# Kernel optimization log

Hardware: AMD Instinct MI355X
Metric: run time of the kernel (lower is better)

Reference implementation:

```python
import jax, jax.numpy as jnp
import numpy as np

B = 4
S = 2_000_000
NPIX = 196608  # 12 * 128**2 (HEALPix nside=128)


def setup_inputs() -> dict:
    key = jax.random.key(0)
    k1, k2, k3, k4 = jax.random.split(key, 4)
    tod = jax.random.normal(k1, (B, S), dtype=jnp.float32)
    # per-sample Stokes weights (I, Q, U) of the pointing matrix rows
    weights = jax.random.normal(k2, (S, 3), dtype=jnp.float32)
    projection_cov = jax.random.uniform(k3, (NPIX,), dtype=jnp.float32)
    pix_idx = jax.random.randint(k4, (S,), 0, NPIX, dtype=jnp.int32)
    return {"tod": tod, "weights": weights, "projection_cov": projection_cov,
            "pix_idx": pix_idx}


def reference(tod, weights, projection_cov, pix_idx):
    npix = projection_cov.shape[0]
    # P^T: scatter-add each TOD sample's Stokes contribution into its pixel.
    # contrib: [B, S, 3]
    contrib = tod[:, :, None] * weights[None, :, :]
    sky = jax.vmap(
        lambda c: jax.ops.segment_sum(c, pix_idx, num_segments=npix)
    )(contrib)  # [B, npix, 3]
    # coverage normalization of I, Q, U
    sky = sky / projection_cov[None, :, None]
    return sky
```

## Files before the change

### kernel.cpp

```cpp
#include <hip/hip_runtime.h>


constexpr int NB   = 768;
constexpr int BW   = 256;
constexpr int NBLK = 512;
constexpr int TILE = 2048;


__device__ __forceinline__ unsigned f2bf(float f) {
    unsigned u = __float_as_uint(f);
    unsigned r = ((u >> 16) & 1u) + 0x7fffu;
    return (u + r) >> 16;
}
__device__ __forceinline__ float bf_lo(unsigned u) {
    return __uint_as_float(u << 16);
}
__device__ __forceinline__ float bf_hi(unsigned u) {
    return __uint_as_float(u & 0xffff0000u);
}


__global__ __launch_bounds__(512)
void hist_kernel(const int* __restrict__ pix, int S, int chunk,
                 int* __restrict__ hist2d) {
    __shared__ int lh[NB];
    for (int t = threadIdx.x; t < NB; t += blockDim.x) lh[t] = 0;
    __syncthreads();
    const int beg = blockIdx.x * chunk;
    const int end = min(S, beg + chunk);
    for (int j = beg + threadIdx.x; j < end; j += blockDim.x)
        atomicAdd(&lh[pix[j] >> 8], 1);
    __syncthreads();
    for (int t = threadIdx.x; t < NB; t += blockDim.x)
        hist2d[(size_t)blockIdx.x * NB + t] = lh[t];
}

__global__ __launch_bounds__(NBLK)
void scan_blocks_kernel(int* __restrict__ hist2d,
                        int* __restrict__ btotal) {
    __shared__ int sc[NBLK];
    const int bkt = blockIdx.x, tid = threadIdx.x;
    const int v = hist2d[(size_t)tid * NB + bkt];
    sc[tid] = v;
    __syncthreads();
    for (int off = 1; off < NBLK; off <<= 1) {
        int x = (tid >= off) ? sc[tid - off] : 0;
        __syncthreads();
        sc[tid] += x;
        __syncthreads();
    }
    hist2d[(size_t)tid * NB + bkt] = sc[tid] - v;
    if (tid == NBLK - 1) btotal[bkt] = sc[tid];
}

__global__ void scan_buckets_kernel(const int* __restrict__ btotal,
                                    int* __restrict__ bbase, int S) {
    __shared__ int sc[NB];
    const int tid = threadIdx.x;
    const int v = btotal[tid];
    sc[tid] = v;
    __syncthreads();
    for (int off = 1; off < NB; off <<= 1) {
        int x = (tid >= off) ? sc[tid - off] : 0;
        __syncthreads();
        sc[tid] += x;
        __syncthreads();
    }
    bbase[tid] = sc[tid] - v;
    if (tid == NB - 1) bbase[NB] = sc[tid];
}

__global__ __launch_bounds__(1024)
void reorder_payload_kernel(const float* __restrict__ tod,
                            const float* __restrict__ weights,
                            const int* __restrict__ pix,
                            int S, int chunk,
                            const int* __restrict__ hist2d,
                            const int* __restrict__ bbase,
                            uint4* __restrict__ rec) {
    __shared__ int lbase[NB];
    __shared__ int lcur[NB];
    const int blk = blockIdx.x;
    for (int t = threadIdx.x; t < NB; t += blockDim.x) {
        lbase[t] = bbase[t] + hist2d[(size_t)blk * NB + t];
        lcur[t] = 0;
    }
    __syncthreads();
    const int beg = blk * chunk;
    const int end = min(S, beg + chunk);
    const int bs  = blockDim.x;

    int j = beg + (int)threadIdx.x;
    int p = 0;
    float w0 = 0, w1 = 0, w2 = 0, t0 = 0, t1 = 0, t2 = 0, t3 = 0;
    if (j < end) {
        p  = pix[j];
        w0 = weights[3 * j + 0]; w1 = weights[3 * j + 1]; w2 = weights[3 * j + 2];
        t0 = tod[(size_t)0 * S + j]; t1 = tod[(size_t)1 * S + j];
        t2 = tod[(size_t)2 * S + j]; t3 = tod[(size_t)3 * S + j];
    }
    while (j < end) {
        const int jn = j + bs;
        int pn = 0;
        float wn0 = 0, wn1 = 0, wn2 = 0, tn0 = 0, tn1 = 0, tn2 = 0, tn3 = 0;
        if (jn < end) {
            pn  = pix[jn];
            wn0 = weights[3 * jn + 0]; wn1 = weights[3 * jn + 1]; wn2 = weights[3 * jn + 2];
            tn0 = tod[(size_t)0 * S + jn]; tn1 = tod[(size_t)1 * S + jn];
            tn2 = tod[(size_t)2 * S + jn]; tn3 = tod[(size_t)3 * S + jn];
        }
        const int bkt = p >> 8;
        const int r   = atomicAdd(&lcur[bkt], 1);
        const int dst = lbase[bkt] + r;
        uint4 v;
        v.x = f2bf(w0) | (f2bf(w1) << 16);
        v.y = f2bf(w2) | ((unsigned)(p & (BW - 1)) << 16);
        v.z = f2bf(t0) | (f2bf(t1) << 16);
        v.w = f2bf(t2) | (f2bf(t3) << 16);
        rec[dst] = v;
        j = jn; p = pn;
        w0 = wn0; w1 = wn1; w2 = wn2;
        t0 = tn0; t1 = tn1; t2 = tn2; t3 = tn3;
    }
}

__global__ __launch_bounds__(1024)
void accum_sort_kernel(const uint4* __restrict__ rec,
                       const float* __restrict__ cov,
                       const int* __restrict__ bbase,
                       float* __restrict__ out,
                       int npix) {
    __shared__ uint4          lrec[TILE];
    __shared__ int            lp[TILE];
    __shared__ unsigned short lidx[TILE];
    __shared__ int            start[BW + 1];
    __shared__ int            cur[BW];

    const int bkt = blockIdx.x;
    const int beg = bbase[bkt], end = bbase[bkt + 1];
    const int l = threadIdx.x & (BW - 1);
    const int q = threadIdx.x >> 8;
    float s0 = 0.f, s1 = 0.f, s2 = 0.f;

    for (int tbeg = beg; tbeg < end; tbeg += TILE) {
        const int n = min(TILE, end - tbeg);

        if (threadIdx.x < BW) cur[threadIdx.x] = 0;
        for (int j = threadIdx.x; j < n; j += blockDim.x) {
            const uint4 r = rec[(size_t)(tbeg + j)];
            lrec[j] = r;
            lp[j]   = (int)(r.y >> 16);
        }
        __syncthreads();

        for (int j = threadIdx.x; j < n; j += blockDim.x)
            atomicAdd(&cur[lp[j]], 1);
        __syncthreads();

        if (threadIdx.x < 64) {
            const int i0 = threadIdx.x * 4;
            const int a0 = cur[i0], a1 = cur[i0 + 1];
            const int a2 = cur[i0 + 2], a3 = cur[i0 + 3];
            const int t1 = a0 + a1, t2 = t1 + a2, t3 = t2 + a3;
            int x = t3;
            #pragma unroll
            for (int off = 1; off < 64; off <<= 1) {
                const int y = __shfl_up(x, off, 64);
                if ((int)threadIdx.x >= off) x += y;
            }
            const int base = x - t3;
            start[i0]     = base;
            start[i0 + 1] = base + a0;
            start[i0 + 2] = base + t1;
            start[i0 + 3] = base + t2;
            if (threadIdx.x == 63) start[BW] = base + t3;
            cur[i0]     = base;
            cur[i0 + 1] = base + a0;
            cur[i0 + 2] = base + t1;
            cur[i0 + 3] = base + t2;
        }
        __syncthreads();

        for (int j = threadIdx.x; j < n; j += blockDim.x) {
            const int r = atomicAdd(&cur[lp[j]], 1);
            lidx[r] = (unsigned short)j;
        }
        __syncthreads();

        const int rb = start[l], re = start[l + 1];
        for (int j = rb; j < re; ++j) {
            const int i = lidx[j];
            const uint4 r = lrec[i];
            float tq;
            if      (q == 0) tq = bf_lo(r.z);
            else if (q == 1) tq = bf_hi(r.z);
            else if (q == 2) tq = bf_lo(r.w);
            else             tq = bf_hi(r.w);
            s0 += tq * bf_lo(r.x);
            s1 += tq * bf_hi(r.x);
            s2 += tq * bf_lo(r.y);
        }
        __syncthreads();
    }

    const int p = bkt * BW + l;
    const float rc = 1.0f / cov[p];
    const size_t o = ((size_t)q * npix + p) * 3;
    out[o + 0] = s0 * rc;
    out[o + 1] = s1 * rc;
    out[o + 2] = s2 * rc;
}


__global__ void zero_out_kernel(float4* __restrict__ out, int n4) {
    int i = blockIdx.x * blockDim.x + threadIdx.x;
    int stride = gridDim.x * blockDim.x;
    for (; i < n4; i += stride) out[i] = make_float4(0.f, 0.f, 0.f, 0.f);
}

__global__ void scatter_kernel(const float* __restrict__ tod,
                               const float* __restrict__ weights,
                               const int*   __restrict__ pix,
                               float* __restrict__ out,
                               int S, int npix, int B) {
    int i = blockIdx.x * blockDim.x + threadIdx.x;
    int stride = gridDim.x * blockDim.x;
    const size_t bstride = (size_t)npix * 3;
    for (int s = i; s < S; s += stride) {
        const int p = pix[s];
        const float w0 = weights[3 * s + 0];
        const float w1 = weights[3 * s + 1];
        const float w2 = weights[3 * s + 2];
        float* o = out + (size_t)p * 3;
        for (int b = 0; b < B; ++b) {
            const float t = tod[(size_t)b * S + s];
            float* ob = o + (size_t)b * bstride;
            atomicAdd(ob + 0, t * w0);
            atomicAdd(ob + 1, t * w1);
            atomicAdd(ob + 2, t * w2);
        }
    }
}

__global__ void normalize_kernel(float* __restrict__ out,
                                 const float* __restrict__ cov,
                                 int npix, int B) {
    int i = blockIdx.x * blockDim.x + threadIdx.x;
    int stride = gridDim.x * blockDim.x;
    const int total = B * npix;
    for (; i < total; i += stride) {
        const int p = i % npix;
        const float c = cov[p];
        float* o = out + (size_t)i * 3;
        o[0] /= c; o[1] /= c; o[2] /= c;
    }
}


extern "C" void kernel_launch(void* const* d_in, const int* in_sizes, int n_in,
                              void* d_out, int out_size, void* d_ws, size_t ws_size,
                              hipStream_t stream) {
    const float* tod     = (const float*)d_in[0];
    const float* weights = (const float*)d_in[1];
    const float* cov     = (const float*)d_in[2];
    const int*   pix     = (const int*)d_in[3];
    float* out = (float*)d_out;

    const int S    = in_sizes[3];
    const int npix = in_sizes[2];
    const int B    = in_sizes[0] / S;

    const size_t meta_ints  = (size_t)NB * NBLK + NB + (NB + 1);
    const size_t meta_bytes = ((meta_ints * sizeof(int)) + 63) & ~(size_t)63;
    const size_t need_rec   = meta_bytes + (size_t)S * 16;

    const int chunk = (S + NBLK - 1) / NBLK;

    if (B == 4 && npix == NB * BW && ws_size >= need_rec) {
        int* hist2d = (int*)d_ws;
        int* btotal = hist2d + (size_t)NB * NBLK;
        int* bbase  = btotal + NB;
        uint4* rec  = (uint4*)((char*)d_ws + meta_bytes);

        hist_kernel<<<NBLK, 512, 0, stream>>>(pix, S, chunk, hist2d);
        scan_blocks_kernel<<<NB, NBLK, 0, stream>>>(hist2d, btotal);
        scan_buckets_kernel<<<1, NB, 0, stream>>>(btotal, bbase, S);
        reorder_payload_kernel<<<NBLK, 1024, 0, stream>>>(tod, weights, pix, S,
                                                          chunk, hist2d, bbase, rec);
        accum_sort_kernel<<<NB, 1024, 0, stream>>>(rec, cov, bbase, out, npix);
        return;
    }

    const int block = 256;
    {
        const int n4 = out_size / 4;
        int grid = min((n4 + block - 1) / block, 2048);
        zero_out_kernel<<<grid, block, 0, stream>>>((float4*)out, n4);
    }
    {
        int grid = min((S + block - 1) / block, 4096);
        scatter_kernel<<<grid, block, 0, stream>>>(tod, weights, pix, out, S, npix, B);
    }
    {
        const int total = B * npix;
        int grid = min((total + block - 1) / block, 2048);
        normalize_kernel<<<grid, block, 0, stream>>>(out, cov, npix, B);
    }
}
```

Baseline: 72.99 us.

## Use wider pixel buckets and locally sort records before global scatter

Buckets change from 768×256 pixels to 256×768 pixels, and the number of reorder chunks doubles to 1024, each at most one TILE. The reorder kernel now stages each chunk's bf16 records in LDS and counting-sorts them by bucket, so writes to the global record array come out as contiguous runs rather than scattered 16-byte stores. The accumulate kernel handles 768 pixels per block, with each thread owning three pixel slots and a 12-wide prefix scan. The cost is only 256 accumulate blocks, which reduces parallelism, plus extra LDS passes in the reorder step and a larger hist2d to scan.

```diff
diff --git a/kernel.cpp b/kernel.cpp
--- a/kernel.cpp
+++ b/kernel.cpp
@@ -1,9 +1,9 @@
 #include <hip/hip_runtime.h>
 
 
-constexpr int NB   = 768;
-constexpr int BW   = 256;
-constexpr int NBLK = 512;
+constexpr int NB   = 256;
+constexpr int BW   = 768;
+constexpr int NBLK = 1024;
 constexpr int TILE = 2048;
 
 
@@ -29,7 +29,7 @@
     const int beg = blockIdx.x * chunk;
     const int end = min(S, beg + chunk);
     for (int j = beg + threadIdx.x; j < end; j += blockDim.x)
-        atomicAdd(&lh[pix[j] >> 8], 1);
+        atomicAdd(&lh[pix[j] / BW], 1);
     __syncthreads();
     for (int t = threadIdx.x; t < NB; t += blockDim.x)
         hist2d[(size_t)blockIdx.x * NB + t] = lh[t];
@@ -53,8 +53,9 @@
     if (tid == NBLK - 1) btotal[bkt] = sc[tid];
 }
 
-__global__ void scan_buckets_kernel(const int* __restrict__ btotal,
-                                    int* __restrict__ bbase, int S) {
+__global__ __launch_bounds__(NB)
+void scan_buckets_kernel(const int* __restrict__ btotal,
+                         int* __restrict__ bbase, int S) {
     __shared__ int sc[NB];
     const int tid = threadIdx.x;
     const int v = btotal[tid];
@@ -70,57 +71,90 @@
     if (tid == NB - 1) bbase[NB] = sc[tid];
 }
 
-__global__ __launch_bounds__(1024)
-void reorder_payload_kernel(const float* __restrict__ tod,
-                            const float* __restrict__ weights,
-                            const int* __restrict__ pix,
-                            int S, int chunk,
-                            const int* __restrict__ hist2d,
-                            const int* __restrict__ bbase,
-                            uint4* __restrict__ rec) {
-    __shared__ int lbase[NB];
-    __shared__ int lcur[NB];
+__global__ __launch_bounds__(512)
+void reorder_sorted_kernel(const float* __restrict__ tod,
+                           const float* __restrict__ weights,
+                           const int* __restrict__ pix,
+                           int S, int chunk,
+                           const int* __restrict__ hist2d,
+                           const int* __restrict__ bbase,
+                           uint4* __restrict__ rec) {
+    __shared__ uint4          lrec[TILE];
+    __shared__ unsigned short lbk[TILE];
+    __shared__ unsigned short lidx[TILE];
+    __shared__ int            lcur[NB];
+    __shared__ int            lstart[NB];
+    __shared__ int            lbase[NB];
+
     const int blk = blockIdx.x;
-    for (int t = threadIdx.x; t < NB; t += blockDim.x) {
-        lbase[t] = bbase[t] + hist2d[(size_t)blk * NB + t];
-        lcur[t] = 0;
-    }
-    __syncthreads();
     const int beg = blk * chunk;
     const int end = min(S, beg + chunk);
-    const int bs  = blockDim.x;
-
-    int j = beg + (int)threadIdx.x;
-    int p = 0;
-    float w0 = 0, w1 = 0, w2 = 0, t0 = 0, t1 = 0, t2 = 0, t3 = 0;
-    if (j < end) {
-        p  = pix[j];
-        w0 = weights[3 * j + 0]; w1 = weights[3 * j + 1]; w2 = weights[3 * j + 2];
-        t0 = tod[(size_t)0 * S + j]; t1 = tod[(size_t)1 * S + j];
-        t2 = tod[(size_t)2 * S + j]; t3 = tod[(size_t)3 * S + j];
-    }
-    while (j < end) {
-        const int jn = j + bs;
-        int pn = 0;
-        float wn0 = 0, wn1 = 0, wn2 = 0, tn0 = 0, tn1 = 0, tn2 = 0, tn3 = 0;
-        if (jn < end) {
-            pn  = pix[jn];
-            wn0 = weights[3 * jn + 0]; wn1 = weights[3 * jn + 1]; wn2 = weights[3 * jn + 2];
-            tn0 = tod[(size_t)0 * S + jn]; tn1 = tod[(size_t)1 * S + jn];
-            tn2 = tod[(size_t)2 * S + jn]; tn3 = tod[(size_t)3 * S + jn];
-        }
-        const int bkt = p >> 8;
-        const int r   = atomicAdd(&lcur[bkt], 1);
-        const int dst = lbase[bkt] + r;
+    const int n = end - beg;
+
+    if (threadIdx.x < NB) {
+        lcur[threadIdx.x] = 0;
+        lbase[threadIdx.x] = bbase[threadIdx.x]
+                           + hist2d[(size_t)blk * NB + threadIdx.x];
+    }
+    __syncthreads();
+
+    for (int jj = threadIdx.x; jj < n; jj += blockDim.x) {
+        const int j = beg + jj;
+        const int p = pix[j];
+        const int bkt = p / BW;
+        const int lp  = p - bkt * BW;
+        const float w0 = weights[3 * j + 0];
+        const float w1 = weights[3 * j + 1];
+        const float w2 = weights[3 * j + 2];
+        const float t0 = tod[(size_t)0 * S + j];
+        const float t1 = tod[(size_t)1 * S + j];
+        const float t2 = tod[(size_t)2 * S + j];
+        const float t3 = tod[(size_t)3 * S + j];
         uint4 v;
         v.x = f2bf(w0) | (f2bf(w1) << 16);
-        v.y = f2bf(w2) | ((unsigned)(p & (BW - 1)) << 16);
+        v.y = f2bf(w2) | ((unsigned)lp << 16);
         v.z = f2bf(t0) | (f2bf(t1) << 16);
         v.w = f2bf(t2) | (f2bf(t3) << 16);
-        rec[dst] = v;
-        j = jn; p = pn;
-        w0 = wn0; w1 = wn1; w2 = wn2;
-        t0 = tn0; t1 = tn1; t2 = tn2; t3 = tn3;
+        lrec[jj] = v;
+        lbk[jj] = (unsigned short)bkt;
+        atomicAdd(&lcur[bkt], 1);
+    }
+    __syncthreads();
+
+    if (threadIdx.x < 64) {
+        const int i0 = threadIdx.x * 4;
+        const int a0 = lcur[i0], a1 = lcur[i0 + 1];
+        const int a2 = lcur[i0 + 2], a3 = lcur[i0 + 3];
+        const int t1 = a0 + a1, t2 = t1 + a2, t3 = t2 + a3;
+        int x = t3;
+        #pragma unroll
+        for (int off = 1; off < 64; off <<= 1) {
+            const int y = __shfl_up(x, off, 64);
+            if ((int)threadIdx.x >= off) x += y;
+        }
+        const int base = x - t3;
+        lstart[i0]     = base;
+        lstart[i0 + 1] = base + a0;
+        lstart[i0 + 2] = base + t1;
+        lstart[i0 + 3] = base + t2;
+        lcur[i0]     = base;
+        lcur[i0 + 1] = base + a0;
+        lcur[i0 + 2] = base + t1;
+        lcur[i0 + 3] = base + t2;
+    }
+    __syncthreads();
+
+    for (int jj = threadIdx.x; jj < n; jj += blockDim.x) {
+        const int r = atomicAdd(&lcur[lbk[jj]], 1);
+        lidx[r] = (unsigned short)jj;
+    }
+    __syncthreads();
+
+    for (int r = threadIdx.x; r < n; r += blockDim.x) {
+        const int jj = lidx[r];
+        const int bkt = lbk[jj];
+        const int dst = lbase[bkt] + (r - lstart[bkt]);
+        rec[dst] = lrec[jj];
     }
 }
 
@@ -131,84 +165,119 @@
                        float* __restrict__ out,
                        int npix) {
     __shared__ uint4          lrec[TILE];
-    __shared__ int            lp[TILE];
+    __shared__ unsigned short lpx[TILE];
     __shared__ unsigned short lidx[TILE];
     __shared__ int            start[BW + 1];
     __shared__ int            cur[BW];
 
     const int bkt = blockIdx.x;
     const int beg = bbase[bkt], end = bbase[bkt + 1];
-    const int l = threadIdx.x & (BW - 1);
+    const int l = threadIdx.x & 255;
     const int q = threadIdx.x >> 8;
-    float s0 = 0.f, s1 = 0.f, s2 = 0.f;
+    float s00 = 0.f, s01 = 0.f, s02 = 0.f;
+    float s10 = 0.f, s11 = 0.f, s12 = 0.f;
+    float s20 = 0.f, s21 = 0.f, s22 = 0.f;
 
     for (int tbeg = beg; tbeg < end; tbeg += TILE) {
         const int n = min(TILE, end - tbeg);
 
-        if (threadIdx.x < BW) cur[threadIdx.x] = 0;
+        for (int t = threadIdx.x; t < BW; t += blockDim.x) cur[t] = 0;
+        __syncthreads();
         for (int j = threadIdx.x; j < n; j += blockDim.x) {
             const uint4 r = rec[(size_t)(tbeg + j)];
             lrec[j] = r;
-            lp[j]   = (int)(r.y >> 16);
-        }
-        __syncthreads();
-
-        for (int j = threadIdx.x; j < n; j += blockDim.x)
-            atomicAdd(&cur[lp[j]], 1);
+            const int lp = (int)(r.y >> 16);
+            lpx[j] = (unsigned short)lp;
+            atomicAdd(&cur[lp], 1);
+        }
         __syncthreads();
 
         if (threadIdx.x < 64) {
-            const int i0 = threadIdx.x * 4;
-            const int a0 = cur[i0], a1 = cur[i0 + 1];
-            const int a2 = cur[i0 + 2], a3 = cur[i0 + 3];
-            const int t1 = a0 + a1, t2 = t1 + a2, t3 = t2 + a3;
-            int x = t3;
+            const int i0 = threadIdx.x * 12;
+            int v[12], pre[12], run = 0;
+            #pragma unroll
+            for (int k = 0; k < 12; ++k) {
+                v[k] = cur[i0 + k]; pre[k] = run; run += v[k];
+            }
+            int x = run;
             #pragma unroll
             for (int off = 1; off < 64; off <<= 1) {
                 const int y = __shfl_up(x, off, 64);
                 if ((int)threadIdx.x >= off) x += y;
             }
-            const int base = x - t3;
-            start[i0]     = base;
-            start[i0 + 1] = base + a0;
-            start[i0 + 2] = base + t1;
-            start[i0 + 3] = base + t2;
-            if (threadIdx.x == 63) start[BW] = base + t3;
-            cur[i0]     = base;
-            cur[i0 + 1] = base + a0;
-            cur[i0 + 2] = base + t1;
-            cur[i0 + 3] = base + t2;
+            const int base = x - run;
+            #pragma unroll
+            for (int k = 0; k < 12; ++k) {
+                start[i0 + k] = base + pre[k];
+                cur[i0 + k]   = base + pre[k];
+            }
+            if (threadIdx.x == 63) start[BW] = base + run;
         }
         __syncthreads();
 
         for (int j = threadIdx.x; j < n; j += blockDim.x) {
-            const int r = atomicAdd(&cur[lp[j]], 1);
+            const int r = atomicAdd(&cur[lpx[j]], 1);
             lidx[r] = (unsigned short)j;
         }
         __syncthreads();
 
-        const int rb = start[l], re = start[l + 1];
-        for (int j = rb; j < re; ++j) {
-            const int i = lidx[j];
-            const uint4 r = lrec[i];
-            float tq;
-            if      (q == 0) tq = bf_lo(r.z);
-            else if (q == 1) tq = bf_hi(r.z);
-            else if (q == 2) tq = bf_lo(r.w);
-            else             tq = bf_hi(r.w);
-            s0 += tq * bf_lo(r.x);
-            s1 += tq * bf_hi(r.x);
-            s2 += tq * bf_lo(r.y);
-        }
-        __syncthreads();
-    }
-
-    const int p = bkt * BW + l;
-    const float rc = 1.0f / cov[p];
-    const size_t o = ((size_t)q * npix + p) * 3;
-    out[o + 0] = s0 * rc;
-    out[o + 1] = s1 * rc;
-    out[o + 2] = s2 * rc;
+        {
+            const int rb = start[l], re = start[l + 1];
+            for (int j = rb; j < re; ++j) {
+                const int i = lidx[j];
+                const uint4 r = lrec[i];
+                const float tq = (q == 0) ? bf_lo(r.z) : (q == 1) ? bf_hi(r.z)
+                               : (q == 2) ? bf_lo(r.w) : bf_hi(r.w);
+                s00 += tq * bf_lo(r.x);
+                s01 += tq * bf_hi(r.x);
+                s02 += tq * bf_lo(r.y);
+            }
+        }
+        {
+            const int rb = start[l + 256], re = start[l + 257];
+            for (int j = rb; j < re; ++j) {
+                const int i = lidx[j];
+                const uint4 r = lrec[i];
+                const float tq = (q == 0) ? bf_lo(r.z) : (q == 1) ? bf_hi(r.z)
+                               : (q == 2) ? bf_lo(r.w) : bf_hi(r.w);
+                s10 += tq * bf_lo(r.x);
+                s11 += tq * bf_hi(r.x);
+                s12 += tq * bf_lo(r.y);
+            }
+        }
+        {
+            const int rb = start[l + 512], re = start[l + 513];
+            for (int j = rb; j < re; ++j) {
+                const int i = lidx[j];
+                const uint4 r = lrec[i];
+                const float tq = (q == 0) ? bf_lo(r.z) : (q == 1) ? bf_hi(r.z)
+                               : (q == 2) ? bf_lo(r.w) : bf_hi(r.w);
+                s20 += tq * bf_lo(r.x);
+                s21 += tq * bf_hi(r.x);
+                s22 += tq * bf_lo(r.y);
+            }
+        }
+        __syncthreads();
+    }
+
+    {
+        const int p = bkt * BW + l;
+        const float rc = 1.0f / cov[p];
+        const size_t o = ((size_t)q * npix + p) * 3;
+        out[o + 0] = s00 * rc; out[o + 1] = s01 * rc; out[o + 2] = s02 * rc;
+    }
+    {
+        const int p = bkt * BW + 256 + l;
+        const float rc = 1.0f / cov[p];
+        const size_t o = ((size_t)q * npix + p) * 3;
+        out[o + 0] = s10 * rc; out[o + 1] = s11 * rc; out[o + 2] = s12 * rc;
+    }
+    {
+        const int p = bkt * BW + 512 + l;
+        const float rc = 1.0f / cov[p];
+        const size_t o = ((size_t)q * npix + p) * 3;
+        out[o + 0] = s20 * rc; out[o + 1] = s21 * rc; out[o + 2] = s22 * rc;
+    }
 }
 
 
@@ -276,7 +345,7 @@
 
     const int chunk = (S + NBLK - 1) / NBLK;
 
-    if (B == 4 && npix == NB * BW && ws_size >= need_rec) {
+    if (B == 4 && npix == NB * BW && chunk <= TILE && ws_size >= need_rec) {
         int* hist2d = (int*)d_ws;
         int* btotal = hist2d + (size_t)NB * NBLK;
         int* bbase  = btotal + NB;
@@ -285,8 +354,8 @@
         hist_kernel<<<NBLK, 512, 0, stream>>>(pix, S, chunk, hist2d);
         scan_blocks_kernel<<<NB, NBLK, 0, stream>>>(hist2d, btotal);
         scan_buckets_kernel<<<1, NB, 0, stream>>>(btotal, bbase, S);
-        reorder_payload_kernel<<<NBLK, 1024, 0, stream>>>(tod, weights, pix, S,
-                                                          chunk, hist2d, bbase, rec);
+        reorder_sorted_kernel<<<NBLK, 512, 0, stream>>>(tod, weights, pix, S,
+                                                        chunk, hist2d, bbase, rec);
         accum_sort_kernel<<<NB, 1024, 0, stream>>>(rec, cov, bbase, out, npix);
         return;
     }
```

Measured after the change: 73.78 us. Within noise of the previous version (+1.1%).
